# Optimization experiments

Measured on AMD Instinct MI355X. Metric: run time of the kernel, lower is better.

Reference implementation:

```python
import jax, jax.numpy as jnp
import numpy as np

SPAN_W = 8      # fixed span width (tokens per span)
HID = 150       # Score hidden dim (hardcoded in source)


def _score_mlp(x, w1, b1, w2, b2, w3, b3):
    # Linear->ReLU->(Dropout=id)->Linear->ReLU->(Dropout=id)->Linear ; out dim 1
    h = jax.nn.relu(x @ w1 + b1)
    h = jax.nn.relu(h @ w2 + b2)
    return h @ w3 + b3


def _make_mlp_params(key, in_dim):
    ks = jax.random.split(key, 6)
    s1 = 1.0 / np.sqrt(in_dim)
    s2 = 1.0 / np.sqrt(HID)
    return (
        jax.random.uniform(ks[0], (in_dim, HID), jnp.float32, -s1, s1),
        jax.random.uniform(ks[1], (HID,), jnp.float32, -s1, s1),
        jax.random.uniform(ks[2], (HID, HID), jnp.float32, -s2, s2),
        jax.random.uniform(ks[3], (HID,), jnp.float32, -s2, s2),
        jax.random.uniform(ks[4], (HID, 1), jnp.float32, -s2, s2),
        jax.random.uniform(ks[5], (1,), jnp.float32, -s2, s2),
    )


def setup_inputs() -> dict:
    key = jax.random.key(0)
    k_emb, k_sp, k_a, k_m, k_p = jax.random.split(key, 5)
    E = 768
    B, T, S = 2, 2048, 96
    encoded_docs = jax.random.normal(k_emb, (B, T, E), jnp.float32)
    span_starts = jnp.sort(
        jax.random.randint(k_sp, (B, S), 0, 2040, dtype=jnp.int64), axis=-1)
    aw1, ab1, aw2, ab2, aw3, ab3 = _make_mlp_params(k_a, E)          # attn Score
    mw1, mb1, mw2, mb2, mw3, mb3 = _make_mlp_params(k_m, 3 * E)      # mention Score
    pw1, pb1, pw2, pb2, pw3, pb3 = _make_mlp_params(k_p, 9 * E)      # pair Score
    return {
        "encoded_docs": encoded_docs, "span_starts": span_starts,
        "aw1": aw1, "ab1": ab1, "aw2": aw2, "ab2": ab2, "aw3": aw3, "ab3": ab3,
        "mw1": mw1, "mb1": mb1, "mw2": mw2, "mb2": mb2, "mw3": mw3, "mb3": mb3,
        "pw1": pw1, "pb1": pb1, "pw2": pw2, "pb2": pb2, "pw3": pw3, "pb3": pb3,
    }


def reference(encoded_docs, span_starts,
              aw1, ab1, aw2, ab2, aw3, ab3,
              mw1, mb1, mw2, mb2, mw3, mb3,
              pw1, pb1, pw2, pb2, pw3, pb3):
    B, T, E = encoded_docs.shape
    S = span_starts.shape[1]

    # --- MentionScore ---
    attns = _score_mlp(encoded_docs, aw1, ab1, aw2, ab2, aw3, ab3)  # [B,T,1]
    starts = span_starts                                              # [B,S]
    ends = starts + (SPAN_W - 1)
    g_start = jnp.take_along_axis(encoded_docs, starts[:, :, None], axis=1)  # [B,S,E]
    g_end = jnp.take_along_axis(encoded_docs, ends[:, :, None], axis=1)      # [B,S,E]
    tok_idx = starts[:, :, None] + jnp.arange(SPAN_W, dtype=starts.dtype)     # [B,S,W]
    flat = tok_idx.reshape(B, S * SPAN_W)
    span_emb = jnp.take_along_axis(encoded_docs, flat[:, :, None], axis=1).reshape(B, S, SPAN_W, E)
    span_attn = jnp.take_along_axis(attns, flat[:, :, None], axis=1).reshape(B, S, SPAN_W, 1)
    g_attn = jnp.sum(span_emb * span_attn, axis=2)                    # [B,S,E]
    g_i = jnp.concatenate([g_start, g_end, g_attn], axis=-1)          # [B,S,3E]
    mention_scores = _score_mlp(g_i, mw1, mb1, mw2, mb2, mw3, mb3)    # [B,S,1]

    # --- PairwiseScore: all pairs (i=span_1, j=span_2) ---
    gi = jnp.broadcast_to(g_i[:, :, None, :], (B, S, S, 3 * E))
    gj = jnp.broadcast_to(g_i[:, None, :, :], (B, S, S, 3 * E))
    pair = jnp.concatenate([gi, gj, gi * gj], axis=-1)                # [B,S,S,9E]
    pair_scores = _score_mlp(pair, pw1, pb1, pw2, pb2, pw3, pb3)      # [B,S,S,1]
    ext = (mention_scores[:, :, None, :] + mention_scores[:, None, :, :] + pair_scores) / 3.0
    return jnp.clip(ext, 0.0, 1.0)
```

## Files before the change

### kernel.cpp

```cpp
#include <hip/hip_runtime.h>

#define EDIM   768
#define E3     2304
#define HIDD   150
#define TT     2048
#define SS     96
#define BB     2

typedef unsigned short u16;
using frag   = __attribute__((ext_vector_type(8))) short;
using f32x4v = __attribute__((ext_vector_type(4))) float;
using u16x8  = __attribute__((ext_vector_type(8))) unsigned short;

__device__ __forceinline__ u16 bf16rn(float f) {
    union { float f; unsigned u; } v; v.f = f;
    unsigned r = v.u + 0x7FFF + ((v.u >> 16) & 1);
    return (u16)(r >> 16);
}
__device__ __forceinline__ float bf16tof(u16 h) {
    union { unsigned u; float f; } v; v.u = ((unsigned)h) << 16;
    return v.f;
}
__device__ __forceinline__ void split2(float f, u16& hi, u16& lo) {
    hi = bf16rn(f); lo = bf16rn(f - bf16tof(hi));
}
__device__ __forceinline__ int swzoff(int row, int qd) {
    return row * 32 + (((qd + (row >> 1)) & 3) << 3);
}

__global__ __launch_bounds__(256) void k_prep_all(
    const float* __restrict__ pw1, const float* __restrict__ mw1,
    const float* __restrict__ aw1, const float* __restrict__ aw2,
    const float* __restrict__ pw2,
    u16* __restrict__ W12t_hi, u16* __restrict__ W12t_lo,
    u16* __restrict__ AW1t_hi, u16* __restrict__ AW1t_lo,
    u16* __restrict__ AW2t_hi, u16* __restrict__ AW2t_lo,
    u16* __restrict__ PW2t_hi, u16* __restrict__ PW2t_lo)
{
    __shared__ float tile[64][33];
    const int bi = blockIdx.x;
    const int t  = threadIdx.x;

    if (bi < 720) {
        const int k0 = (bi % 36) * 64;
        const int n0 = (bi / 36) * 32;
        const int seg = n0 / 160;
        const int nloc0 = n0 - seg * 160;
        for (int idx = t; idx < 2048; idx += 256) {
            const int kk = idx >> 5, nn = idx & 31;
            const int nl = nloc0 + nn;
            const int k  = k0 + kk;
            float v = 0.f;
            if (nl < HIDD) {
                if (seg == 0)      v = pw1[(long)k * HIDD + nl];
                else if (seg == 1) v = pw1[(long)(E3 + k) * HIDD + nl];
                else if (seg == 2) v = mw1[(long)k * HIDD + nl];
                else               v = pw1[(long)(2 * E3 + k) * HIDD + nl];
            }
            tile[kk][nn] = v;
        }
        __syncthreads();
        for (int idx = t; idx < 2048; idx += 256) {
            const int nn = idx >> 6, kk = idx & 63;
            u16 hi, lo; split2(tile[kk][nn], hi, lo);
            W12t_hi[(long)(n0 + nn) * E3 + k0 + kk] = hi;
            W12t_lo[(long)(n0 + nn) * E3 + k0 + kk] = lo;
        }
    } else if (bi < 1488) {
        const int k = bi - 720;
        if (t < 160) {
            float v = (t < HIDD) ? aw1[k * HIDD + t] : 0.f;
            u16 hi, lo; split2(v, hi, lo);
            AW1t_hi[(long)t * EDIM + k] = hi;
            AW1t_lo[(long)t * EDIM + k] = lo;
        }
    } else {
        const int r = bi - 1488;
        const int k = r % 160;
        const int which = r / 160;
        const float* src = which ? pw2 : aw2;
        u16* dh = which ? PW2t_hi : AW2t_hi;
        u16* dl = which ? PW2t_lo : AW2t_lo;
        if (t < 160) {
            float v = (t < HIDD && k < HIDD) ? src[k * HIDD + t] : 0.f;
            u16 hi, lo; split2(v, hi, lo);
            dh[t * 160 + k] = hi;
            dl[t * 160 + k] = lo;
        }
    }
}

__global__ __launch_bounds__(256) void k_attn1(
    const float* __restrict__ X, const int* __restrict__ spans,
    const u16* __restrict__ AW1t_hi, const u16* __restrict__ AW1t_lo,
    float* __restrict__ AH1)
{
    __shared__ __align__(16) u16 As_hi[32 * 40];
    __shared__ __align__(16) u16 As_lo[32 * 40];
    __shared__ __align__(16) u16 Bs_hi[160 * 40];
    __shared__ __align__(16) u16 Bs_lo[160 * 40];

    const int t    = threadIdx.x;
    const int lane = t & 63;
    const int m    = lane & 15;
    const int quad = lane >> 4;
    const int w    = t >> 6;
    const int mt   = (w & 1) * 16;
    const int nb   = (w >> 1) * 80;
    const int ks   = blockIdx.y;

    const int rr = t >> 3, q = t & 7;
    const int grow = blockIdx.x * 32 + rr;
    const int bs = grow >> 3, sw = grow & 7;
    const int b  = bs / SS;
    const int tok = spans[bs] + sw;
    const float* arow = X + ((long)b * TT + tok) * EDIM;

    f32x4v acc[5];
    #pragma unroll
    for (int ht = 0; ht < 5; ++ht)
        #pragma unroll
        for (int r = 0; r < 4; ++r) acc[ht][r] = 0.f;

    for (int tt = 0; tt < 6; ++tt) {
        const int kk0 = ks * 192 + tt * 32;
        {
            const float4 xv = *(const float4*)&arow[kk0 + q * 4];
            ushort4 hv, lv;
            split2(xv.x, hv.x, lv.x); split2(xv.y, hv.y, lv.y);
            split2(xv.z, hv.z, lv.z); split2(xv.w, hv.w, lv.w);
            *(ushort4*)&As_hi[rr * 40 + q * 4] = hv;
            *(ushort4*)&As_lo[rr * 40 + q * 4] = lv;
        }
        #pragma unroll
        for (int it = 0; it < 3; ++it) {
            const int v = t + it * 256;
            if (v < 640) {
                const int h = v >> 2, qq = v & 3;
                *(uint4*)&Bs_hi[h * 40 + qq * 8] = *(const uint4*)&AW1t_hi[(long)h * EDIM + kk0 + qq * 8];
                *(uint4*)&Bs_lo[h * 40 + qq * 8] = *(const uint4*)&AW1t_lo[(long)h * EDIM + kk0 + qq * 8];
            }
        }
        __syncthreads();
        const frag ah = *(const frag*)&As_hi[(mt + m) * 40 + quad * 8];
        const frag al = *(const frag*)&As_lo[(mt + m) * 40 + quad * 8];
        #pragma unroll
        for (int ht = 0; ht < 5; ++ht) {
            const frag bh = *(const frag*)&Bs_hi[(nb + ht * 16 + m) * 40 + quad * 8];
            const frag bl = *(const frag*)&Bs_lo[(nb + ht * 16 + m) * 40 + quad * 8];
            acc[ht] = __builtin_amdgcn_mfma_f32_16x16x32_bf16(al, bh, acc[ht], 0, 0, 0);
            acc[ht] = __builtin_amdgcn_mfma_f32_16x16x32_bf16(ah, bl, acc[ht], 0, 0, 0);
            acc[ht] = __builtin_amdgcn_mfma_f32_16x16x32_bf16(ah, bh, acc[ht], 0, 0, 0);
        }
        __syncthreads();
    }
    #pragma unroll
    for (int ht = 0; ht < 5; ++ht) {
        #pragma unroll
        for (int r = 0; r < 4; ++r) {
            const int row = blockIdx.x * 32 + mt + quad * 4 + r;
            const int col = nb + ht * 16 + m;
            if (col < HIDD) atomicAdd(&AH1[row * 160 + col], acc[ht][r]);
        }
    }
}

__global__ __launch_bounds__(256) void k_attn2(
    const float* __restrict__ AH1,
    const u16* __restrict__ AW2t_hi, const u16* __restrict__ AW2t_lo,
    const float* __restrict__ ab1, const float* __restrict__ ab2,
    const float* __restrict__ aw3, const float* __restrict__ ab3,
    float* __restrict__ attn_g)
{
    __shared__ __align__(16) u16 As_hi[32 * 40];
    __shared__ __align__(16) u16 As_lo[32 * 40];
    __shared__ __align__(16) u16 Bs_hi[160 * 40];
    __shared__ __align__(16) u16 Bs_lo[160 * 40];
    __shared__ float h1s[32 * 160];
    __shared__ float red[32];

    const int t    = threadIdx.x;
    const int lane = t & 63;
    const int m    = lane & 15;
    const int quad = lane >> 4;
    const int w    = t >> 6;
    const int mt   = (w & 1) * 16;
    const int nb   = (w >> 1) * 80;

    for (int u = t; u < 1280; u += 256) {
        const int row = u / 40, c4 = u - (u / 40) * 40;
        const int c0 = c4 * 4;
        const float4 v = *(const float4*)&AH1[(blockIdx.x * 32 + row) * 160 + c0];
        h1s[row * 160 + c0 + 0] = (c0 + 0 < HIDD) ? fmaxf(v.x + ab1[c0 + 0], 0.f) : 0.f;
        h1s[row * 160 + c0 + 1] = (c0 + 1 < HIDD) ? fmaxf(v.y + ab1[c0 + 1], 0.f) : 0.f;
        h1s[row * 160 + c0 + 2] = (c0 + 2 < HIDD) ? fmaxf(v.z + ab1[c0 + 2], 0.f) : 0.f;
        h1s[row * 160 + c0 + 3] = (c0 + 3 < HIDD) ? fmaxf(v.w + ab1[c0 + 3], 0.f) : 0.f;
    }
    if (t < 32) red[t] = 0.f;
    __syncthreads();

    const int rr = t >> 3, q = t & 7;
    f32x4v acc2[5];
    #pragma unroll
    for (int ht = 0; ht < 5; ++ht)
        #pragma unroll
        for (int r = 0; r < 4; ++r) acc2[ht][r] = 0.f;

    for (int kk = 0; kk < 5; ++kk) {
        {
            const float4 xv = *(const float4*)&h1s[rr * 160 + kk * 32 + q * 4];
            ushort4 hv, lv;
            split2(xv.x, hv.x, lv.x); split2(xv.y, hv.y, lv.y);
            split2(xv.z, hv.z, lv.z); split2(xv.w, hv.w, lv.w);
            *(ushort4*)&As_hi[rr * 40 + q * 4] = hv;
            *(ushort4*)&As_lo[rr * 40 + q * 4] = lv;
        }
        #pragma unroll
        for (int it = 0; it < 3; ++it) {
            const int v = t + it * 256;
            if (v < 640) {
                const int h = v >> 2, qq = v & 3;
                *(uint4*)&Bs_hi[h * 40 + qq * 8] = *(const uint4*)&AW2t_hi[h * 160 + kk * 32 + qq * 8];
                *(uint4*)&Bs_lo[h * 40 + qq * 8] = *(const uint4*)&AW2t_lo[h * 160 + kk * 32 + qq * 8];
            }
        }
        __syncthreads();
        const frag ah = *(const frag*)&As_hi[(mt + m) * 40 + quad * 8];
        const frag al = *(const frag*)&As_lo[(mt + m) * 40 + quad * 8];
        #pragma unroll
        for (int ht = 0; ht < 5; ++ht) {
            const frag bh = *(const frag*)&Bs_hi[(nb + ht * 16 + m) * 40 + quad * 8];
            const frag bl = *(const frag*)&Bs_lo[(nb + ht * 16 + m) * 40 + quad * 8];
            acc2[ht] = __builtin_amdgcn_mfma_f32_16x16x32_bf16(al, bh, acc2[ht], 0, 0, 0);
            acc2[ht] = __builtin_amdgcn_mfma_f32_16x16x32_bf16(ah, bl, acc2[ht], 0, 0, 0);
            acc2[ht] = __builtin_amdgcn_mfma_f32_16x16x32_bf16(ah, bh, acc2[ht], 0, 0, 0);
        }
        __syncthreads();
    }

    float s[4] = {0.f, 0.f, 0.f, 0.f};
    #pragma unroll
    for (int ht = 0; ht < 5; ++ht) {
        const int col = nb + ht * 16 + m;
        if (col < HIDD) {
            const float w3 = aw3[col];
            #pragma unroll
            for (int r = 0; r < 4; ++r)
                s[r] += fmaxf(acc2[ht][r] + ab2[col], 0.f) * w3;
        }
    }
    #pragma unroll
    for (int r = 0; r < 4; ++r) {
        for (int off = 8; off > 0; off >>= 1) s[r] += __shfl_down(s[r], off, 16);
    }
    if (m == 0) {
        #pragma unroll
        for (int r = 0; r < 4; ++r) atomicAdd(&red[mt + quad * 4 + r], s[r]);
    }
    __syncthreads();
    if (t < 32) attn_g[blockIdx.x * 32 + t] = red[t] + ab3[0];
}

__global__ __launch_bounds__(256) void k_span_g(
    const float* __restrict__ X, const int* __restrict__ spans,
    const float* __restrict__ attn_g, float* __restrict__ G_ws,
    u16* __restrict__ Gs_hi, u16* __restrict__ Gs_lo)
{
    __shared__ float a8[8];
    const int t  = threadIdx.x;
    const int bs = blockIdx.x;
    const int b  = bs / SS;
    const int start = spans[bs];
    const float* xb = X + ((long)b * TT + start) * EDIM;
    float* Gp = G_ws + (long)bs * E3;
    u16* Gh = Gs_hi + (long)bs * E3;
    u16* Gl = Gs_lo + (long)bs * E3;
    if (t < 8) a8[t] = attn_g[bs * 8 + t];
    __syncthreads();

    for (int e = t; e < EDIM; e += 256) {
        const float gs = xb[e];
        const float ge = xb[7 * EDIM + e];
        float ga = 0.f;
        #pragma unroll
        for (int w = 0; w < 8; ++w) ga += xb[w * EDIM + e] * a8[w];
        Gp[e] = gs; Gp[EDIM + e] = ge; Gp[2 * EDIM + e] = ga;
        u16 hi, lo;
        split2(gs, hi, lo); Gh[e] = hi;            Gl[e] = lo;
        split2(ge, hi, lo); Gh[EDIM + e] = hi;     Gl[EDIM + e] = lo;
        split2(ga, hi, lo); Gh[2 * EDIM + e] = hi; Gl[2 * EDIM + e] = lo;
    }
}

__global__ __launch_bounds__(256) void k_uvm(
    const u16* __restrict__ Gs_hi, const u16* __restrict__ Gs_lo,
    const u16* __restrict__ W9t_hi, const u16* __restrict__ W9t_lo,
    float* __restrict__ UVM)
{
    __shared__ __align__(16) u16 As_hi[64 * 40];
    __shared__ __align__(16) u16 As_lo[64 * 40];
    __shared__ __align__(16) u16 Bs_hi[160 * 40];
    __shared__ __align__(16) u16 Bs_lo[160 * 40];

    const int t    = threadIdx.x;
    const int mb   = blockIdx.x;
    const int nb   = blockIdx.y;
    const int ks   = blockIdx.z;
    const int lane = t & 63;
    const int m    = lane & 15;
    const int quad = lane >> 4;
    const int w    = t >> 6;
    const int mhalf = (w & 1) * 32;
    const int nbase = (w >> 1) * 80;
    const int arr = t >> 2, aq = t & 3;

    f32x4v acc[2][5];
    #pragma unroll
    for (int i = 0; i < 2; ++i)
        #pragma unroll
        for (int j = 0; j < 5; ++j)
            #pragma unroll
            for (int r = 0; r < 4; ++r) acc[i][j][r] = 0.f;

    for (int tt = 0; tt < 6; ++tt) {
        const int kk0 = ks * 192 + tt * 32;
        *(uint4*)&As_hi[arr * 40 + aq * 8] = *(const uint4*)&Gs_hi[(long)(mb * 64 + arr) * E3 + kk0 + aq * 8];
        *(uint4*)&As_lo[arr * 40 + aq * 8] = *(const uint4*)&Gs_lo[(long)(mb * 64 + arr) * E3 + kk0 + aq * 8];
        #pragma unroll
        for (int it = 0; it < 3; ++it) {
            const int v = t + it * 256;
            if (v < 640) {
                const int h = v >> 2, qq = v & 3;
                *(uint4*)&Bs_hi[h * 40 + qq * 8] = *(const uint4*)&W9t_hi[(long)(nb * 160 + h) * E3 + kk0 + qq * 8];
                *(uint4*)&Bs_lo[h * 40 + qq * 8] = *(const uint4*)&W9t_lo[(long)(nb * 160 + h) * E3 + kk0 + qq * 8];
            }
        }
        __syncthreads();
        frag ah[2], al[2];
        #pragma unroll
        for (int mt = 0; mt < 2; ++mt) {
            ah[mt] = *(const frag*)&As_hi[(mhalf + mt * 16 + m) * 40 + quad * 8];
            al[mt] = *(const frag*)&As_lo[(mhalf + mt * 16 + m) * 40 + quad * 8];
        }
        #pragma unroll
        for (int ht = 0; ht < 5; ++ht) {
            const frag bh = *(const frag*)&Bs_hi[(nbase + ht * 16 + m) * 40 + quad * 8];
            const frag bl = *(const frag*)&Bs_lo[(nbase + ht * 16 + m) * 40 + quad * 8];
            #pragma unroll
            for (int mt = 0; mt < 2; ++mt) {
                acc[mt][ht] = __builtin_amdgcn_mfma_f32_16x16x32_bf16(al[mt], bh, acc[mt][ht], 0, 0, 0);
                acc[mt][ht] = __builtin_amdgcn_mfma_f32_16x16x32_bf16(ah[mt], bl, acc[mt][ht], 0, 0, 0);
                acc[mt][ht] = __builtin_amdgcn_mfma_f32_16x16x32_bf16(ah[mt], bh, acc[mt][ht], 0, 0, 0);
            }
        }
        __syncthreads();
    }
    float* dst = UVM + (long)nb * (192 * 160);
    #pragma unroll
    for (int mt = 0; mt < 2; ++mt) {
        #pragma unroll
        for (int ht = 0; ht < 5; ++ht) {
            #pragma unroll
            for (int r = 0; r < 4; ++r) {
                const int row = mb * 64 + mhalf + mt * 16 + quad * 4 + r;
                const int c   = nbase + ht * 16 + m;
                atomicAdd(&dst[row * 160 + c], acc[mt][ht][r]);
            }
        }
    }
}

__global__ __launch_bounds__(256) void k_mention(
    const float* __restrict__ M_ws,
    const float* __restrict__ mb1,
    const float* __restrict__ mw2, const float* __restrict__ mb2,
    const float* __restrict__ mw3, const float* __restrict__ mb3,
    float* __restrict__ m_ws)
{
    __shared__ float h1m[152];
    __shared__ float h2m[152];
    __shared__ float red[256];
    const int t  = threadIdx.x;
    const int bs = blockIdx.x;
    if (t < HIDD) h1m[t] = fmaxf(M_ws[bs * 160 + t] + mb1[t], 0.f);
    __syncthreads();
    if (t < HIDD) {
        float a = mb2[t];
        for (int k = 0; k < HIDD; ++k) a += h1m[k] * mw2[k * HIDD + t];
        h2m[t] = fmaxf(a, 0.f);
    }
    __syncthreads();
    red[t] = (t < HIDD) ? h2m[t] * mw3[t] : 0.f;
    __syncthreads();
    for (int off = 128; off > 0; off >>= 1) {
        if (t < off) red[t] += red[t + off];
        __syncthreads();
    }
    if (t == 0) m_ws[bs] = red[0] + mb3[0];
}

__global__ __launch_bounds__(256) void k_pairmm(
    const float* __restrict__ G_ws,
    const u16* __restrict__ PCt_hi, const u16* __restrict__ PCt_lo,
    float* __restrict__ H1)
{
    __shared__ float gis[384];
    __shared__ __align__(16) u16 As_hi[96 * 32];
    __shared__ __align__(16) u16 As_lo[96 * 32];
    __shared__ __align__(16) u16 Bs_hi[160 * 32];
    __shared__ __align__(16) u16 Bs_lo[160 * 32];

    const int t  = threadIdx.x;
    const int ks = blockIdx.x;
    const int i  = blockIdx.y;
    const int b  = blockIdx.z;
    const int ksbase = ks * 384;
    const int jt0 = i >> 4;
    const int ntiles = 6 - jt0;
    const int j0 = jt0 * 16;
    const int R  = 96 - j0;

    const int lane = t & 63;
    const int m    = lane & 15;
    const int quad = lane >> 4;
    const int w    = t >> 6;
    const int hb   = (w & 1) * 80;
    const int apar = w >> 1;

    const float* Gi = G_ws + (long)(b * SS + i) * E3 + ksbase;
    for (int e = t; e < 384; e += 256) gis[e] = Gi[e];
    __syncthreads();

    f32x4v acc[3][5];
    #pragma unroll
    for (int jt = 0; jt < 3; ++jt)
        #pragma unroll
        for (int ht = 0; ht < 5; ++ht)
            #pragma unroll
            for (int r = 0; r < 4; ++r) acc[jt][ht][r] = 0.f;

    for (int tt = 0; tt < 12; ++tt) {
        const int kk0 = ksbase + tt * 32;
        for (int u = t; u < R * 4; u += 256) {
            const int rr = u >> 2, qd = u & 3;
            const float* gj = &G_ws[(long)(b * SS + j0 + rr) * E3 + kk0 + qd * 8];
            const float4 g0 = *(const float4*)&gj[0];
            const float4 g1 = *(const float4*)&gj[4];
            const int kl = tt * 32 + qd * 8;
            u16x8 hv, lv; u16 h, l;
            split2(g0.x * gis[kl + 0], h, l); hv[0] = h; lv[0] = l;
            split2(g0.y * gis[kl + 1], h, l); hv[1] = h; lv[1] = l;
            split2(g0.z * gis[kl + 2], h, l); hv[2] = h; lv[2] = l;
            split2(g0.w * gis[kl + 3], h, l); hv[3] = h; lv[3] = l;
            split2(g1.x * gis[kl + 4], h, l); hv[4] = h; lv[4] = l;
            split2(g1.y * gis[kl + 5], h, l); hv[5] = h; lv[5] = l;
            split2(g1.z * gis[kl + 6], h, l); hv[6] = h; lv[6] = l;
            split2(g1.w * gis[kl + 7], h, l); hv[7] = h; lv[7] = l;
            const int o = swzoff(rr, qd);
            *(u16x8*)&As_hi[o] = hv;
            *(u16x8*)&As_lo[o] = lv;
        }
        for (int v = t; v < 640; v += 256) {
            const int h = v >> 2, qd = v & 3;
            const int o = swzoff(h, qd);
            *(uint4*)&Bs_hi[o] = *(const uint4*)&PCt_hi[(long)h * E3 + kk0 + qd * 8];
            *(uint4*)&Bs_lo[o] = *(const uint4*)&PCt_lo[(long)h * E3 + kk0 + qd * 8];
        }
        __syncthreads();
        frag ah[3], al[3];
        #pragma unroll
        for (int u = 0; u < 3; ++u) {
            const int a = apar + 2 * u;
            if (a < ntiles) {
                const int o = swzoff(a * 16 + m, quad);
                ah[u] = *(const frag*)&As_hi[o];
                al[u] = *(const frag*)&As_lo[o];
            }
        }
        #pragma unroll
        for (int ht = 0; ht < 5; ++ht) {
            const int o = swzoff(hb + ht * 16 + m, quad);
            const frag bh = *(const frag*)&Bs_hi[o];
            const frag bl = *(const frag*)&Bs_lo[o];
            #pragma unroll
            for (int u = 0; u < 3; ++u) {
                if (apar + 2 * u < ntiles) {
                    acc[u][ht] = __builtin_amdgcn_mfma_f32_16x16x32_bf16(al[u], bh, acc[u][ht], 0, 0, 0);
                    acc[u][ht] = __builtin_amdgcn_mfma_f32_16x16x32_bf16(ah[u], bl, acc[u][ht], 0, 0, 0);
                    acc[u][ht] = __builtin_amdgcn_mfma_f32_16x16x32_bf16(ah[u], bh, acc[u][ht], 0, 0, 0);
                }
            }
        }
        __syncthreads();
    }

    #pragma unroll
    for (int u = 0; u < 3; ++u) {
        const int a = apar + 2 * u;
        if (a < ntiles) {
            #pragma unroll
            for (int ht = 0; ht < 5; ++ht) {
                #pragma unroll
                for (int r = 0; r < 4; ++r) {
                    const int j = (jt0 + a) * 16 + quad * 4 + r;
                    const int h = hb + ht * 16 + m;
                    atomicAdd(&H1[((long)(b * SS + i) * SS + j) * 160 + h], acc[u][ht][r]);
                }
            }
        }
    }
}

__global__ __launch_bounds__(256) void k_pair2(
    const float* __restrict__ H1,
    const float* __restrict__ U_ws, const float* __restrict__ V_ws,
    const float* __restrict__ pb1, const float* __restrict__ m_ws,
    const u16* __restrict__ PW2t_hi, const u16* __restrict__ PW2t_lo,
    const float* __restrict__ pb2, const float* __restrict__ pw3,
    const float* __restrict__ pb3,
    float* __restrict__ out)
{
    __shared__ __align__(16) u16 As_hi[96 * 168];
    __shared__ __align__(16) u16 As_lo[96 * 168];
    __shared__ __align__(16) u16 Bs_hi[160 * 40];
    __shared__ __align__(16) u16 Bs_lo[160 * 40];
    __shared__ float uv[160];
    __shared__ float red[96];

    const int t  = threadIdx.x;
    const int bi = blockIdx.x;
    const int b  = bi / SS;
    const int ii = bi - b * SS;

    if (t < 160) uv[t] = U_ws[bi * 160 + t] + ((t < HIDD) ? pb1[t] : 0.f);
    if (t < 96) red[t] = 0.f;
    __syncthreads();

    for (int u = t; u < 96 * 40; u += 256) {
        const int j = u / 40, hq = u - (u / 40) * 40;
        const int h0 = hq * 4;
        const int mn = ii < j ? ii : j;
        const int mx = ii < j ? j : ii;
        const long idx = (((long)b * SS + mn) * SS + mx) * 160 + h0;
        const float4 a  = *(const float4*)&H1[idx];
        const float4 vv = *(const float4*)&V_ws[(b * SS + j) * 160 + h0];
        const float p0 = fmaxf(a.x + vv.x + uv[h0 + 0], 0.f);
        const float p1 = fmaxf(a.y + vv.y + uv[h0 + 1], 0.f);
        const float p2 = fmaxf(a.z + vv.z + uv[h0 + 2], 0.f);
        const float p3 = fmaxf(a.w + vv.w + uv[h0 + 3], 0.f);
        ushort4 hv, lv;
        split2(p0, hv.x, lv.x); split2(p1, hv.y, lv.y);
        split2(p2, hv.z, lv.z); split2(p3, hv.w, lv.w);
        *(ushort4*)&As_hi[j * 168 + h0] = hv;
        *(ushort4*)&As_lo[j * 168 + h0] = lv;
    }
    __syncthreads();

    const int lane = t & 63;
    const int m    = lane & 15;
    const int quad = lane >> 4;
    const int w    = t >> 6;
    const int jbs  = (w & 1) * 48;
    const int nbs  = (w >> 1) * 80;

    f32x4v acc[3][5];
    #pragma unroll
    for (int jt = 0; jt < 3; ++jt)
        #pragma unroll
        for (int ht = 0; ht < 5; ++ht)
            #pragma unroll
            for (int r = 0; r < 4; ++r) acc[jt][ht][r] = 0.f;

    for (int kk = 0; kk < 5; ++kk) {
        #pragma unroll
        for (int it = 0; it < 3; ++it) {
            const int v = t + it * 256;
            if (v < 640) {
                const int n = v >> 2, qq = v & 3;
                *(uint4*)&Bs_hi[n * 40 + qq * 8] = *(const uint4*)&PW2t_hi[n * 160 + kk * 32 + qq * 8];
                *(uint4*)&Bs_lo[n * 40 + qq * 8] = *(const uint4*)&PW2t_lo[n * 160 + kk * 32 + qq * 8];
            }
        }
        __syncthreads();
        frag ah[3], al[3];
        #pragma unroll
        for (int jt = 0; jt < 3; ++jt) {
            ah[jt] = *(const frag*)&As_hi[(jbs + jt * 16 + m) * 168 + kk * 32 + quad * 8];
            al[jt] = *(const frag*)&As_lo[(jbs + jt * 16 + m) * 168 + kk * 32 + quad * 8];
        }
        #pragma unroll
        for (int ht = 0; ht < 5; ++ht) {
            const frag bh = *(const frag*)&Bs_hi[(nbs + ht * 16 + m) * 40 + quad * 8];
            const frag bl = *(const frag*)&Bs_lo[(nbs + ht * 16 + m) * 40 + quad * 8];
            #pragma unroll
            for (int jt = 0; jt < 3; ++jt) {
                acc[jt][ht] = __builtin_amdgcn_mfma_f32_16x16x32_bf16(al[jt], bh, acc[jt][ht], 0, 0, 0);
                acc[jt][ht] = __builtin_amdgcn_mfma_f32_16x16x32_bf16(ah[jt], bl, acc[jt][ht], 0, 0, 0);
                acc[jt][ht] = __builtin_amdgcn_mfma_f32_16x16x32_bf16(ah[jt], bh, acc[jt][ht], 0, 0, 0);
            }
        }
        __syncthreads();
    }

    float s[3][4];
    #pragma unroll
    for (int jt = 0; jt < 3; ++jt)
        #pragma unroll
        for (int r = 0; r < 4; ++r) s[jt][r] = 0.f;
    #pragma unroll
    for (int ht = 0; ht < 5; ++ht) {
        const int col = nbs + ht * 16 + m;
        if (col < HIDD) {
            const float w3 = pw3[col];
            const float b2 = pb2[col];
            #pragma unroll
            for (int jt = 0; jt < 3; ++jt)
                #pragma unroll
                for (int r = 0; r < 4; ++r)
                    s[jt][r] += fmaxf(acc[jt][ht][r] + b2, 0.f) * w3;
        }
    }
    #pragma unroll
    for (int jt = 0; jt < 3; ++jt)
        #pragma unroll
        for (int r = 0; r < 4; ++r)
            for (int off = 8; off > 0; off >>= 1)
                s[jt][r] += __shfl_down(s[jt][r], off, 16);
    if (m == 0) {
        #pragma unroll
        for (int jt = 0; jt < 3; ++jt)
            #pragma unroll
            for (int r = 0; r < 4; ++r)
                atomicAdd(&red[jbs + jt * 16 + quad * 4 + r], s[jt][r]);
    }
    __syncthreads();

    if (t < 96) {
        const float sc = red[t] + pb3[0];
        const float v = (m_ws[bi] + m_ws[b * SS + t] + sc) * (1.f / 3.f);
        out[(long)bi * SS + t] = fminf(fmaxf(v, 0.f), 1.f);
    }
}

extern "C" void kernel_launch(void* const* d_in, const int* in_sizes, int n_in,
                              void* d_out, int out_size, void* d_ws, size_t ws_size,
                              hipStream_t stream)
{
    const float* X     = (const float*)d_in[0];
    const int*   spans = (const int*)  d_in[1];
    const float* aw1 = (const float*)d_in[2];
    const float* ab1 = (const float*)d_in[3];
    const float* aw2 = (const float*)d_in[4];
    const float* ab2 = (const float*)d_in[5];
    const float* aw3 = (const float*)d_in[6];
    const float* ab3 = (const float*)d_in[7];
    const float* mw1 = (const float*)d_in[8];
    const float* mb1 = (const float*)d_in[9];
    const float* mw2 = (const float*)d_in[10];
    const float* mb2 = (const float*)d_in[11];
    const float* mw3 = (const float*)d_in[12];
    const float* mb3 = (const float*)d_in[13];
    const float* pw1 = (const float*)d_in[14];
    const float* pb1 = (const float*)d_in[15];
    const float* pw2 = (const float*)d_in[16];
    const float* pb2 = (const float*)d_in[17];
    const float* pw3 = (const float*)d_in[18];
    const float* pb3 = (const float*)d_in[19];
    float* out = (float*)d_out;

    char* p = (char*)d_ws;
    float* attn_g  = (float*)p;  p += 6144;
    float* G_ws    = (float*)p;  p += (long)442368 * 4;
    u16*   Gs_hi   = (u16*)p;    p += (long)442368 * 2;
    u16*   Gs_lo   = (u16*)p;    p += (long)442368 * 2;
    float* UVM     = (float*)p;  p += (long)3 * 192 * 160 * 4;
    float* AH1     = (float*)p;  p += (long)1536 * 160 * 4;
    float* m_ws    = (float*)p;  p += 1024;
    u16*   W12t_hi = (u16*)p;    p += (long)640 * E3 * 2;
    u16*   W12t_lo = (u16*)p;    p += (long)640 * E3 * 2;
    u16*   AW1t_hi = (u16*)p;    p += (long)160 * EDIM * 2;
    u16*   AW1t_lo = (u16*)p;    p += (long)160 * EDIM * 2;
    u16*   AW2t_hi = (u16*)p;    p += 160 * 160 * 2;
    u16*   AW2t_lo = (u16*)p;    p += 160 * 160 * 2;
    u16*   PW2t_hi = (u16*)p;    p += 160 * 160 * 2;
    u16*   PW2t_lo = (u16*)p;    p += 160 * 160 * 2;
    float* H1      = (float*)p;

    float* U_ws = UVM;
    float* V_ws = UVM + 192 * 160;
    float* M_ws = UVM + 2 * 192 * 160;
    const u16* PCt_hi = W12t_hi + (long)480 * E3;
    const u16* PCt_lo = W12t_lo + (long)480 * E3;

    hipMemsetAsync(UVM, 0, ((size_t)3 * 192 * 160 + (size_t)1536 * 160) * sizeof(float), stream);
    hipMemsetAsync(H1, 0, (size_t)192 * SS * 160 * sizeof(float), stream);

    k_prep_all<<<dim3(1808), 256, 0, stream>>>(pw1, mw1, aw1, aw2, pw2,
                                               W12t_hi, W12t_lo, AW1t_hi, AW1t_lo,
                                               AW2t_hi, AW2t_lo, PW2t_hi, PW2t_lo);

    k_attn1<<<dim3(48, 4), 256, 0, stream>>>(X, spans, AW1t_hi, AW1t_lo, AH1);
    k_attn2<<<dim3(48), 256, 0, stream>>>(AH1, AW2t_hi, AW2t_lo, ab1, ab2, aw3, ab3, attn_g);
    k_span_g<<<dim3(BB * SS), 256, 0, stream>>>(X, spans, attn_g, G_ws, Gs_hi, Gs_lo);
    k_uvm<<<dim3(3, 3, 12), 256, 0, stream>>>(Gs_hi, Gs_lo, W12t_hi, W12t_lo, UVM);
    k_mention<<<dim3(BB * SS), 256, 0, stream>>>(M_ws, mb1, mw2, mb2, mw3, mb3, m_ws);
    k_pairmm<<<dim3(6, SS, BB), 256, 0, stream>>>(G_ws, PCt_hi, PCt_lo, H1);
    k_pair2<<<dim3(BB * SS), 256, 0, stream>>>(
        H1, U_ws, V_ws, pb1, m_ws, PW2t_hi, PW2t_lo, pb2, pw3, pb3, out);
}
```

Before: 243.5 us.

## Replace atomic split-K in pair matmul with partial buffers and async LDS loads

The pair GEMM now uses 3 K-slices of 768 instead of 6 of 384. Each slice writes plain stores into its own partial H1 buffer, and the second pair kernel sums the three buffers. This removes the H1 memset and the atomicAdd traffic. Weight tiles and G_j rows are now staged into LDS with global_load_lds async copies instead of loads through registers. The cost is fewer blocks in the grid, three times the partial-buffer memory, and extra reads in k_pair2.

```diff
diff --git a/kernel.cpp b/kernel.cpp
--- a/kernel.cpp
+++ b/kernel.cpp
@@ -26,6 +26,11 @@
 }
 __device__ __forceinline__ int swzoff(int row, int qd) {
     return row * 32 + (((qd + (row >> 1)) & 3) << 3);
+}
+__device__ __forceinline__ void async16(const void* g, void* l) {
+    __builtin_amdgcn_global_load_lds(
+        (const __attribute__((address_space(1))) void*)g,
+        (__attribute__((address_space(3))) void*)l, 16, 0, 0);
 }
 
 __global__ __launch_bounds__(256) void k_prep_all(
@@ -402,9 +407,10 @@
 __global__ __launch_bounds__(256) void k_pairmm(
     const float* __restrict__ G_ws,
     const u16* __restrict__ PCt_hi, const u16* __restrict__ PCt_lo,
-    float* __restrict__ H1)
-{
-    __shared__ float gis[384];
+    float* __restrict__ H1parts)
+{
+    __shared__ float gis[768];
+    __shared__ __align__(16) float gjst[96 * 32];
     __shared__ __align__(16) u16 As_hi[96 * 32];
     __shared__ __align__(16) u16 As_lo[96 * 32];
     __shared__ __align__(16) u16 Bs_hi[160 * 32];
@@ -414,11 +420,12 @@
     const int ks = blockIdx.x;
     const int i  = blockIdx.y;
     const int b  = blockIdx.z;
-    const int ksbase = ks * 384;
+    const int ksbase = ks * 768;
     const int jt0 = i >> 4;
     const int ntiles = 6 - jt0;
     const int j0 = jt0 * 16;
     const int R  = 96 - j0;
+    const int nI = R >> 3;
 
     const int lane = t & 63;
     const int m    = lane & 15;
@@ -427,9 +434,13 @@
     const int hb   = (w & 1) * 80;
     const int apar = w >> 1;
 
+    const int Bl_h  = lane >> 2;
+    const int Bl_c  = lane & 3;
+    const int gj_r  = lane >> 3;
+    const int gj_c  = lane & 7;
+
     const float* Gi = G_ws + (long)(b * SS + i) * E3 + ksbase;
-    for (int e = t; e < 384; e += 256) gis[e] = Gi[e];
-    __syncthreads();
+    for (int e = t; e < 768; e += 256) gis[e] = Gi[e];
 
     f32x4v acc[3][5];
     #pragma unroll
@@ -439,13 +450,26 @@
             #pragma unroll
             for (int r = 0; r < 4; ++r) acc[jt][ht][r] = 0.f;
 
-    for (int tt = 0; tt < 12; ++tt) {
+    for (int tt = 0; tt < 24; ++tt) {
         const int kk0 = ksbase + tt * 32;
+        for (int q2 = w; q2 < 10; q2 += 4) {
+            const int h  = q2 * 16 + Bl_h;
+            const int qd = (Bl_c - (h >> 1)) & 3;
+            const long so = (long)h * E3 + kk0 + qd * 8;
+            async16(&PCt_hi[so], &Bs_hi[q2 * 512]);
+            async16(&PCt_lo[so], &Bs_lo[q2 * 512]);
+        }
+        for (int g2 = w; g2 < nI; g2 += 4) {
+            const int row = j0 + g2 * 8 + gj_r;
+            async16(&G_ws[(long)(b * SS + row) * E3 + kk0 + gj_c * 4],
+                    &gjst[g2 * 256]);
+        }
+        __syncthreads();
+
         for (int u = t; u < R * 4; u += 256) {
             const int rr = u >> 2, qd = u & 3;
-            const float* gj = &G_ws[(long)(b * SS + j0 + rr) * E3 + kk0 + qd * 8];
-            const float4 g0 = *(const float4*)&gj[0];
-            const float4 g1 = *(const float4*)&gj[4];
+            const float4 g0 = *(const float4*)&gjst[rr * 32 + qd * 8];
+            const float4 g1 = *(const float4*)&gjst[rr * 32 + qd * 8 + 4];
             const int kl = tt * 32 + qd * 8;
             u16x8 hv, lv; u16 h, l;
             split2(g0.x * gis[kl + 0], h, l); hv[0] = h; lv[0] = l;
@@ -460,13 +484,8 @@
             *(u16x8*)&As_hi[o] = hv;
             *(u16x8*)&As_lo[o] = lv;
         }
-        for (int v = t; v < 640; v += 256) {
-            const int h = v >> 2, qd = v & 3;
-            const int o = swzoff(h, qd);
-            *(uint4*)&Bs_hi[o] = *(const uint4*)&PCt_hi[(long)h * E3 + kk0 + qd * 8];
-            *(uint4*)&Bs_lo[o] = *(const uint4*)&PCt_lo[(long)h * E3 + kk0 + qd * 8];
-        }
-        __syncthreads();
+        __syncthreads();
+
         frag ah[3], al[3];
         #pragma unroll
         for (int u = 0; u < 3; ++u) {
@@ -494,6 +513,7 @@
         __syncthreads();
     }
 
+    float* dst = H1parts + (long)ks * ((long)BB * SS * SS * 160);
     #pragma unroll
     for (int u = 0; u < 3; ++u) {
         const int a = apar + 2 * u;
@@ -504,7 +524,7 @@
                 for (int r = 0; r < 4; ++r) {
                     const int j = (jt0 + a) * 16 + quad * 4 + r;
                     const int h = hb + ht * 16 + m;
-                    atomicAdd(&H1[((long)(b * SS + i) * SS + j) * 160 + h], acc[u][ht][r]);
+                    dst[((long)(b * SS + i) * SS + j) * 160 + h] = acc[u][ht][r];
                 }
             }
         }
@@ -512,7 +532,8 @@
 }
 
 __global__ __launch_bounds__(256) void k_pair2(
-    const float* __restrict__ H1,
+    const float* __restrict__ H1a, const float* __restrict__ H1b,
+    const float* __restrict__ H1c,
     const float* __restrict__ U_ws, const float* __restrict__ V_ws,
     const float* __restrict__ pb1, const float* __restrict__ m_ws,
     const u16* __restrict__ PW2t_hi, const u16* __restrict__ PW2t_lo,
@@ -542,12 +563,14 @@
         const int mn = ii < j ? ii : j;
         const int mx = ii < j ? j : ii;
         const long idx = (((long)b * SS + mn) * SS + mx) * 160 + h0;
-        const float4 a  = *(const float4*)&H1[idx];
+        const float4 a  = *(const float4*)&H1a[idx];
+        const float4 bb = *(const float4*)&H1b[idx];
+        const float4 c  = *(const float4*)&H1c[idx];
         const float4 vv = *(const float4*)&V_ws[(b * SS + j) * 160 + h0];
-        const float p0 = fmaxf(a.x + vv.x + uv[h0 + 0], 0.f);
-        const float p1 = fmaxf(a.y + vv.y + uv[h0 + 1], 0.f);
-        const float p2 = fmaxf(a.z + vv.z + uv[h0 + 2], 0.f);
-        const float p3 = fmaxf(a.w + vv.w + uv[h0 + 3], 0.f);
+        const float p0 = fmaxf(a.x + bb.x + c.x + vv.x + uv[h0 + 0], 0.f);
+        const float p1 = fmaxf(a.y + bb.y + c.y + vv.y + uv[h0 + 1], 0.f);
+        const float p2 = fmaxf(a.z + bb.z + c.z + vv.z + uv[h0 + 2], 0.f);
+        const float p3 = fmaxf(a.w + bb.w + c.w + vv.w + uv[h0 + 3], 0.f);
         ushort4 hv, lv;
         split2(p0, hv.x, lv.x); split2(p1, hv.y, lv.y);
         split2(p2, hv.z, lv.z); split2(p3, hv.w, lv.w);
@@ -684,7 +707,7 @@
     u16*   AW2t_lo = (u16*)p;    p += 160 * 160 * 2;
     u16*   PW2t_hi = (u16*)p;    p += 160 * 160 * 2;
     u16*   PW2t_lo = (u16*)p;    p += 160 * 160 * 2;
-    float* H1      = (float*)p;
+    float* H1parts = (float*)p;
 
     float* U_ws = UVM;
     float* V_ws = UVM + 192 * 160;
@@ -693,7 +716,6 @@
     const u16* PCt_lo = W12t_lo + (long)480 * E3;
 
     hipMemsetAsync(UVM, 0, ((size_t)3 * 192 * 160 + (size_t)1536 * 160) * sizeof(float), stream);
-    hipMemsetAsync(H1, 0, (size_t)192 * SS * 160 * sizeof(float), stream);
 
     k_prep_all<<<dim3(1808), 256, 0, stream>>>(pw1, mw1, aw1, aw2, pw2,
                                                W12t_hi, W12t_lo, AW1t_hi, AW1t_lo,
@@ -704,7 +726,10 @@
     k_span_g<<<dim3(BB * SS), 256, 0, stream>>>(X, spans, attn_g, G_ws, Gs_hi, Gs_lo);
     k_uvm<<<dim3(3, 3, 12), 256, 0, stream>>>(Gs_hi, Gs_lo, W12t_hi, W12t_lo, UVM);
     k_mention<<<dim3(BB * SS), 256, 0, stream>>>(M_ws, mb1, mw2, mb2, mw3, mb3, m_ws);
-    k_pairmm<<<dim3(6, SS, BB), 256, 0, stream>>>(G_ws, PCt_hi, PCt_lo, H1);
+    k_pairmm<<<dim3(3, SS, BB), 256, 0, stream>>>(G_ws, PCt_hi, PCt_lo, H1parts);
+
+    const long H1sz = (long)BB * SS * SS * 160;
     k_pair2<<<dim3(BB * SS), 256, 0, stream>>>(
-        H1, U_ws, V_ws, pb1, m_ws, PW2t_hi, PW2t_lo, pb2, pw3, pb3, out);
-}
+        H1parts, H1parts + H1sz, H1parts + 2 * H1sz,
+        U_ws, V_ws, pb1, m_ws, PW2t_hi, PW2t_lo, pb2, pw3, pb3, out);
+}
```

New measurement: 225.6 us. 1.08x faster.
